# Performance work log

Hardware: AMD Instinct MI355X
Metric: run time of the kernel (lower is better)

## Reference

```python
import jax, jax.numpy as jnp
import numpy as np

B, S, HID = 4, 2048, 1024
NH, IM, E = 4, 2048, 4
EPS = 1e-6


def setup_inputs() -> dict:
    key = jax.random.key(0)
    ks = jax.random.split(key, 12)
    init = lambda k, shape: (jax.random.normal(k, shape, jnp.float32) * 0.02)
    return {
        "hidden_states": jax.random.normal(ks[0], (B, S, HID), jnp.float32),
        "ln1_w": jnp.ones((HID,), jnp.float32),
        "wq": init(ks[1], (HID, HID)),
        "wk": init(ks[2], (HID, HID)),
        "wv": init(ks[3], (HID, HID)),
        "wo": init(ks[4], (HID, HID)),
        "ln2_w": jnp.ones((HID,), jnp.float32),
        "router_w": init(ks[5], (HID, E)),
        "router_b": jnp.zeros((E,), jnp.float32),
        "gate_w": init(ks[6], (E, HID, IM)),
        "up_w": init(ks[7], (E, HID, IM)),
        "down_w": init(ks[8], (E, IM, HID)),
    }


def _rms(x, w):
    return w * (x * jax.lax.rsqrt(jnp.mean(x * x, axis=-1, keepdims=True) + EPS))


def reference(hidden_states, ln1_w, wq, wk, wv, wo, ln2_w,
              router_w, router_b, gate_w, up_w, down_w):
    b, s, h = hidden_states.shape
    nh, d = NH, h // NH

    # ---- attention block (elu+1 feature map, then full softmax) ----
    x = _rms(hidden_states, ln1_w)
    q = (x @ wq).reshape(b, s, nh, d).transpose(0, 2, 1, 3)  # [b,nh,s,d]
    k = (x @ wk).reshape(b, s, nh, d).transpose(0, 2, 1, 3)
    v = (x @ wv).reshape(b, s, nh, d).transpose(0, 2, 1, 3)
    q = jax.nn.elu(q) + 1.0
    k = jax.nn.elu(k) + 1.0
    scores = jnp.einsum('bhqd,bhkd->bhqk', q, k)
    attn = jax.nn.softmax(scores, axis=-1)  # dropout is identity at eval
    o = jnp.einsum('bhqk,bhkd->bhqd', attn, v)
    o = o.transpose(0, 2, 1, 3).reshape(b, s, h) @ wo
    h1 = hidden_states + o

    # ---- MoE block: router softmax, balance loss, dense expert loop ----
    x2 = _rms(h1, ln2_w)
    logits = x2 @ router_w + router_b            # [b,s,E]
    rw = jax.nn.softmax(logits, axis=-1)
    mean_routing = rw.mean(axis=0)               # mean over batch dim only, [s,E]
    balance_loss = jnp.mean((mean_routing - 1.0 / E) ** 2) * 0.01

    # source computes EVERY expert over all tokens, weighted by the FULL
    # softmax routing weight (top-k weights are computed but unused)
    moe_out = jnp.zeros_like(x2)
    for i in range(E):
        g = jax.nn.silu(x2 @ gate_w[i])
        u = x2 @ up_w[i]
        moe_out = moe_out + ((g * u) @ down_w[i]) * rw[..., i:i + 1]

    return h1 + moe_out, balance_loss
```

## Files before the change

### kernel.cpp

```cpp
#include <hip/hip_runtime.h>
#include <cstdint>
#include <cstddef>

#define B_    4
#define S_    2048
#define HID_  1024
#define NH_   4
#define HD_   256
#define IM_   2048
#define E_    4
#define M_    8192
#define NHG_  4

typedef __bf16 bf16x8 __attribute__((ext_vector_type(8)));
typedef float  f32x4  __attribute__((ext_vector_type(4)));

__device__ __forceinline__ unsigned short f32_to_bf16(float f) {
  unsigned int u = __float_as_uint(f);
  u += 0x7fffu + ((u >> 16) & 1u);
  return (unsigned short)(u >> 16);
}

__device__ __forceinline__ void gload16(const unsigned short* g, unsigned short* l) {
  __builtin_amdgcn_global_load_lds(
      (const __attribute__((address_space(1))) void*)g,
      (__attribute__((address_space(3))) void*)l, 16, 0, 0);
}

__device__ __forceinline__ void swizzle_xy(int& bx, int& by) {
  const int gx = gridDim.x, gy = gridDim.y;
  const int flat = blockIdx.x + blockIdx.y * gx;
  const int xcd = flat & 7, i = flat >> 3;
  const int rpx = gy >> 3;
  bx = i % gx;
  by = xcd * rpx + i / gx;
}

#define EPI_F32      0
#define EPI_VT       2
#define EPI_PV_O     3
#define EPI_WO       4
#define EPI_DOWN     5

struct EpiAux {
  float* c_f32;
  unsigned short* c_bf16;
  const float* add_src;
  float* out2;
  long long strideCz;
  int ldc;
};

template<int EPI>
__global__ __launch_bounds__(256) void gemm_bf16k(
    const unsigned short* __restrict__ A, int lda, long long sAo, long long sAi, int zbA,
    const unsigned short* __restrict__ B, int ldb, long long sBo, long long sBi, int zbB,
    int zshift, int zmask, int zbC, int K, EpiAux aux)
{
  __shared__ unsigned short As[2][128 * 32];
  __shared__ unsigned short Bs[2][128 * 32];

  const int t = threadIdx.x;
  int bx, by;
  swizzle_xy(bx, by);
  const int m0 = by * 128, n0 = bx * 128;
  const int z  = blockIdx.z;
  const int zA = z + zbA, zB = z + zbB, zC = z + zbC;
  const unsigned short* Ab = A + (long long)(zA >> zshift) * sAo + (long long)(zA & zmask) * sAi;
  const unsigned short* Bb = B + (long long)(zB >> zshift) * sBo + (long long)(zB & zmask) * sBi;

  const int lane = t & 63, wave = t >> 6;
  const int wm = (wave >> 1) * 64, wn = (wave & 1) * 64;
  const int lrow = lane & 15, quad = lane >> 4;

  f32x4 acc[4][4] = {};

  const int srow = lane >> 2;
  const int sko  = (lane & 3) * 8;
  const unsigned short* aRow0 = Ab + (long long)(m0 + wave * 16       + srow) * lda + sko;
  const unsigned short* aRow1 = Ab + (long long)(m0 + (wave + 4) * 16 + srow) * lda + sko;
  const unsigned short* bRow0 = Bb + (long long)(n0 + wave * 16       + srow) * ldb + sko;
  const unsigned short* bRow1 = Bb + (long long)(n0 + (wave + 4) * 16 + srow) * ldb + sko;
  const int dst0 = (wave * 16) * 32, dst1 = ((wave + 4) * 16) * 32;

  gload16(aRow0, &As[0][dst0]);
  gload16(aRow1, &As[0][dst1]);
  gload16(bRow0, &Bs[0][dst0]);
  gload16(bRow1, &Bs[0][dst1]);

  int cur = 0;
  for (int kk = 0; kk < K; kk += 32, cur ^= 1) {
    __syncthreads();
    if (kk + 32 < K) {
      const int nxt = cur ^ 1, k2 = kk + 32;
      gload16(aRow0 + k2, &As[nxt][dst0]);
      gload16(aRow1 + k2, &As[nxt][dst1]);
      gload16(bRow0 + k2, &Bs[nxt][dst0]);
      gload16(bRow1 + k2, &Bs[nxt][dst1]);
    }
    bf16x8 af[4], bfr[4];
    #pragma unroll
    for (int i = 0; i < 4; ++i) {
      af[i]  = *reinterpret_cast<const bf16x8*>(&As[cur][(wm + i * 16 + lrow) * 32 + quad * 8]);
      bfr[i] = *reinterpret_cast<const bf16x8*>(&Bs[cur][(wn + i * 16 + lrow) * 32 + quad * 8]);
    }
    #pragma unroll
    for (int i = 0; i < 4; ++i)
      #pragma unroll
      for (int j = 0; j < 4; ++j)
        acc[i][j] = __builtin_amdgcn_mfma_f32_16x16x32_bf16(af[i], bfr[j], acc[i][j], 0, 0, 0);
  }

  #pragma unroll
  for (int mi = 0; mi < 4; ++mi) {
    #pragma unroll
    for (int ni = 0; ni < 4; ++ni) {
      #pragma unroll
      for (int r = 0; r < 4; ++r) {
        const int gm = m0 + wm + mi * 16 + quad * 4 + r;
        const int gn = n0 + wn + ni * 16 + lrow;
        const float val = acc[mi][ni][r];
        if (EPI == EPI_F32) {
          aux.c_f32[(long long)zC * aux.strideCz + (long long)gm * aux.ldc + gn] = val;
        } else if (EPI == EPI_VT) {
          const int b = gm >> 11, s = gm & (S_ - 1);
          const int h = gn >> 8, d = gn & (HD_ - 1);
          aux.c_bf16[((long long)(b * NH_ + h) * HD_ + d) * S_ + s] = f32_to_bf16(val);
        } else if (EPI == EPI_PV_O) {
          const int b = zC >> 2, h = zC & (NH_ - 1);
          aux.c_bf16[((long long)(b * S_ + gm)) * HID_ + h * HD_ + gn] = f32_to_bf16(val);
        } else if (EPI == EPI_WO) {
          const long long idx = (long long)gm * HID_ + gn;
          aux.out2[idx] = val + aux.add_src[idx];
        } else if (EPI == EPI_DOWN) {
          const long long idx = (long long)gm * HID_ + gn;
          aux.out2[idx] += val;
        }
      }
    }
  }
}

#define EPI2_QK 0
#define EPI2_GU 1

template<int EPI2>
__global__ __launch_bounds__(256, 2) void gemm_dual_k(
    const unsigned short* __restrict__ A,
    const unsigned short* __restrict__ B0b,
    const unsigned short* __restrict__ B1b,
    int zb,
    unsigned short* __restrict__ out0, unsigned short* __restrict__ out1,
    const float* __restrict__ rw)
{
  __shared__ unsigned short As[2][128 * 32];
  __shared__ unsigned short B0s[2][128 * 32];
  __shared__ unsigned short B1s[2][128 * 32];

  const int t = threadIdx.x;
  int bx, by;
  swizzle_xy(bx, by);
  const int m0 = by * 128, n0 = bx * 128;

  const int lane = t & 63, wave = t >> 6;
  const int wm = (wave >> 1) * 64, wn = (wave & 1) * 64;
  const int lrow = lane & 15, quad = lane >> 4;

  f32x4 acc0[4][4] = {}, acc1[4][4] = {};

  const int srow = lane >> 2;
  const int sko  = (lane & 3) * 8;
  const unsigned short* aRow0 = A   + (long long)(m0 + wave * 16       + srow) * HID_ + sko;
  const unsigned short* aRow1 = A   + (long long)(m0 + (wave + 4) * 16 + srow) * HID_ + sko;
  const unsigned short* gRow0 = B0b + (long long)(n0 + wave * 16       + srow) * HID_ + sko;
  const unsigned short* gRow1 = B0b + (long long)(n0 + (wave + 4) * 16 + srow) * HID_ + sko;
  const unsigned short* uRow0 = B1b + (long long)(n0 + wave * 16       + srow) * HID_ + sko;
  const unsigned short* uRow1 = B1b + (long long)(n0 + (wave + 4) * 16 + srow) * HID_ + sko;
  const int dst0 = (wave * 16) * 32, dst1 = ((wave + 4) * 16) * 32;

  gload16(aRow0, &As[0][dst0]);
  gload16(aRow1, &As[0][dst1]);
  gload16(gRow0, &B0s[0][dst0]);
  gload16(gRow1, &B0s[0][dst1]);
  gload16(uRow0, &B1s[0][dst0]);
  gload16(uRow1, &B1s[0][dst1]);

  int cur = 0;
  for (int kk = 0; kk < HID_; kk += 32, cur ^= 1) {
    __syncthreads();
    if (kk + 32 < HID_) {
      const int nxt = cur ^ 1, k2 = kk + 32;
      gload16(aRow0 + k2, &As[nxt][dst0]);
      gload16(aRow1 + k2, &As[nxt][dst1]);
      gload16(gRow0 + k2, &B0s[nxt][dst0]);
      gload16(gRow1 + k2, &B0s[nxt][dst1]);
      gload16(uRow0 + k2, &B1s[nxt][dst0]);
      gload16(uRow1 + k2, &B1s[nxt][dst1]);
    }
    bf16x8 af[4], b0[4], b1[4];
    #pragma unroll
    for (int i = 0; i < 4; ++i) {
      af[i] = *reinterpret_cast<const bf16x8*>(&As[cur][(wm + i * 16 + lrow) * 32 + quad * 8]);
      b0[i] = *reinterpret_cast<const bf16x8*>(&B0s[cur][(wn + i * 16 + lrow) * 32 + quad * 8]);
      b1[i] = *reinterpret_cast<const bf16x8*>(&B1s[cur][(wn + i * 16 + lrow) * 32 + quad * 8]);
    }
    #pragma unroll
    for (int i = 0; i < 4; ++i)
      #pragma unroll
      for (int j = 0; j < 4; ++j) {
        acc0[i][j] = __builtin_amdgcn_mfma_f32_16x16x32_bf16(af[i], b0[j], acc0[i][j], 0, 0, 0);
        acc1[i][j] = __builtin_amdgcn_mfma_f32_16x16x32_bf16(af[i], b1[j], acc1[i][j], 0, 0, 0);
      }
  }

  #pragma unroll
  for (int mi = 0; mi < 4; ++mi)
    #pragma unroll
    for (int r = 0; r < 4; ++r) {
      const int gm = m0 + wm + mi * 16 + quad * 4 + r;
      float rwv = 0.f;
      if (EPI2 == EPI2_GU) rwv = rw[(long long)gm * E_ + zb];
      #pragma unroll
      for (int ni = 0; ni < 4; ++ni) {
        const int gn = n0 + wn + ni * 16 + lrow;
        const float v0 = acc0[mi][ni][r];
        const float v1 = acc1[mi][ni][r];
        if (EPI2 == EPI2_QK) {
          const float eq = v0 > 0.f ? v0 + 1.f : __expf(v0);
          const float ek = v1 > 0.f ? v1 + 1.f : __expf(v1);
          out0[(long long)gm * HID_ + gn] = f32_to_bf16(eq);
          out1[(long long)gm * HID_ + gn] = f32_to_bf16(ek);
        } else {
          const float sg = v0 / (1.f + __expf(-v0));
          out0[(long long)gm * IM_ + gn] = f32_to_bf16(sg * v1 * rwv);
        }
      }
    }
}

__global__ __launch_bounds__(256, 2) void gemm_down2_k(
    const unsigned short* __restrict__ A0,
    const unsigned short* __restrict__ A1,
    const unsigned short* __restrict__ B0,
    const unsigned short* __restrict__ B1,
    float* __restrict__ out)
{
  __shared__ unsigned short A0s[2][128 * 32];
  __shared__ unsigned short A1s[2][128 * 32];
  __shared__ unsigned short B0s[2][128 * 32];
  __shared__ unsigned short B1s[2][128 * 32];

  const int t = threadIdx.x;
  int bx, by;
  swizzle_xy(bx, by);
  const int m0 = by * 128, n0 = bx * 128;

  const int lane = t & 63, wave = t >> 6;
  const int wm = (wave >> 1) * 64, wn = (wave & 1) * 64;
  const int lrow = lane & 15, quad = lane >> 4;

  f32x4 acc[4][4] = {};

  const int srow = lane >> 2;
  const int sko  = (lane & 3) * 8;
  const unsigned short* a0r0 = A0 + (long long)(m0 + wave * 16       + srow) * IM_ + sko;
  const unsigned short* a0r1 = A0 + (long long)(m0 + (wave + 4) * 16 + srow) * IM_ + sko;
  const unsigned short* a1r0 = A1 + (long long)(m0 + wave * 16       + srow) * IM_ + sko;
  const unsigned short* a1r1 = A1 + (long long)(m0 + (wave + 4) * 16 + srow) * IM_ + sko;
  const unsigned short* b0r0 = B0 + (long long)(n0 + wave * 16       + srow) * IM_ + sko;
  const unsigned short* b0r1 = B0 + (long long)(n0 + (wave + 4) * 16 + srow) * IM_ + sko;
  const unsigned short* b1r0 = B1 + (long long)(n0 + wave * 16       + srow) * IM_ + sko;
  const unsigned short* b1r1 = B1 + (long long)(n0 + (wave + 4) * 16 + srow) * IM_ + sko;
  const int dst0 = (wave * 16) * 32, dst1 = ((wave + 4) * 16) * 32;

  gload16(a0r0, &A0s[0][dst0]);
  gload16(a0r1, &A0s[0][dst1]);
  gload16(a1r0, &A1s[0][dst0]);
  gload16(a1r1, &A1s[0][dst1]);
  gload16(b0r0, &B0s[0][dst0]);
  gload16(b0r1, &B0s[0][dst1]);
  gload16(b1r0, &B1s[0][dst0]);
  gload16(b1r1, &B1s[0][dst1]);

  int cur = 0;
  for (int kk = 0; kk < IM_; kk += 32, cur ^= 1) {
    __syncthreads();
    if (kk + 32 < IM_) {
      const int nxt = cur ^ 1, k2 = kk + 32;
      gload16(a0r0 + k2, &A0s[nxt][dst0]);
      gload16(a0r1 + k2, &A0s[nxt][dst1]);
      gload16(a1r0 + k2, &A1s[nxt][dst0]);
      gload16(a1r1 + k2, &A1s[nxt][dst1]);
      gload16(b0r0 + k2, &B0s[nxt][dst0]);
      gload16(b0r1 + k2, &B0s[nxt][dst1]);
      gload16(b1r0 + k2, &B1s[nxt][dst0]);
      gload16(b1r1 + k2, &B1s[nxt][dst1]);
    }
    bf16x8 a0f[4], a1f[4], b0f[4], b1f[4];
    #pragma unroll
    for (int i = 0; i < 4; ++i) {
      a0f[i] = *reinterpret_cast<const bf16x8*>(&A0s[cur][(wm + i * 16 + lrow) * 32 + quad * 8]);
      a1f[i] = *reinterpret_cast<const bf16x8*>(&A1s[cur][(wm + i * 16 + lrow) * 32 + quad * 8]);
      b0f[i] = *reinterpret_cast<const bf16x8*>(&B0s[cur][(wn + i * 16 + lrow) * 32 + quad * 8]);
      b1f[i] = *reinterpret_cast<const bf16x8*>(&B1s[cur][(wn + i * 16 + lrow) * 32 + quad * 8]);
    }
    #pragma unroll
    for (int i = 0; i < 4; ++i)
      #pragma unroll
      for (int j = 0; j < 4; ++j) {
        acc[i][j] = __builtin_amdgcn_mfma_f32_16x16x32_bf16(a0f[i], b0f[j], acc[i][j], 0, 0, 0);
        acc[i][j] = __builtin_amdgcn_mfma_f32_16x16x32_bf16(a1f[i], b1f[j], acc[i][j], 0, 0, 0);
      }
  }

  #pragma unroll
  for (int mi = 0; mi < 4; ++mi)
    #pragma unroll
    for (int ni = 0; ni < 4; ++ni)
      #pragma unroll
      for (int r = 0; r < 4; ++r) {
        const int gm = m0 + wm + mi * 16 + quad * 4 + r;
        const int gn = n0 + wn + ni * 16 + lrow;
        out[(long long)gm * HID_ + gn] += acc[mi][ni][r];
      }
}

__global__ void transpose_cast4_k(const float* s0, const float* s1,
                                  const float* s2, const float* s3,
                                  unsigned short* __restrict__ out, int R, int C)
{
  __shared__ float tile[32][33];
  const int z = blockIdx.z;
  const float* in = (z == 0) ? s0 : (z == 1) ? s1 : (z == 2) ? s2 : s3;
  unsigned short* o = out + (long long)z * R * C;
  const int c0 = blockIdx.x * 32, r0 = blockIdx.y * 32;
  const int tx = threadIdx.x, ty = threadIdx.y;
  #pragma unroll
  for (int i = 0; i < 32; i += 8)
    tile[ty + i][tx] = in[(long long)(r0 + ty + i) * C + c0 + tx];
  __syncthreads();
  #pragma unroll
  for (int i = 0; i < 32; i += 8)
    o[(long long)(c0 + ty + i) * R + r0 + tx] = f32_to_bf16(tile[tx][ty + i]);
}

__global__ void transpose_cast2x4_k(const float* __restrict__ sA,
                                    const float* __restrict__ sB,
                                    unsigned short* __restrict__ dA,
                                    unsigned short* __restrict__ dB,
                                    int R, int C)
{
  __shared__ float tile[32][33];
  const int z = blockIdx.z;
  const long long eo = (long long)(z & 3) * R * C;
  const float* in = ((z < 4) ? sA : sB) + eo;
  unsigned short* o = ((z < 4) ? dA : dB) + eo;
  const int c0 = blockIdx.x * 32, r0 = blockIdx.y * 32;
  const int tx = threadIdx.x, ty = threadIdx.y;
  #pragma unroll
  for (int i = 0; i < 32; i += 8)
    tile[ty + i][tx] = in[(long long)(r0 + ty + i) * C + c0 + tx];
  __syncthreads();
  #pragma unroll
  for (int i = 0; i < 32; i += 8)
    o[(long long)(c0 + ty + i) * R + r0 + tx] = f32_to_bf16(tile[tx][ty + i]);
}

__global__ void transpose_cast_k(const float* __restrict__ in,
                                 unsigned short* __restrict__ out, int R, int C)
{
  __shared__ float tile[32][33];
  const long long bo = (long long)blockIdx.z * R * C;
  const int c0 = blockIdx.x * 32, r0 = blockIdx.y * 32;
  const int tx = threadIdx.x, ty = threadIdx.y;
  #pragma unroll
  for (int i = 0; i < 32; i += 8)
    tile[ty + i][tx] = in[bo + (long long)(r0 + ty + i) * C + c0 + tx];
  __syncthreads();
  #pragma unroll
  for (int i = 0; i < 32; i += 8)
    out[bo + (long long)(c0 + ty + i) * R + r0 + tx] = f32_to_bf16(tile[tx][ty + i]);
}

__global__ __launch_bounds__(256) void rmsnorm_cast_k(
    const float* __restrict__ x, const float* __restrict__ w,
    unsigned short* __restrict__ out)
{
  __shared__ float red[4];
  const int row = blockIdx.x, t = threadIdx.x;
  const float4 v = reinterpret_cast<const float4*>(x + (long long)row * HID_)[t];
  float ss = v.x * v.x + v.y * v.y + v.z * v.z + v.w * v.w;
  #pragma unroll
  for (int off = 32; off > 0; off >>= 1) ss += __shfl_down(ss, off, 64);
  if ((t & 63) == 0) red[t >> 6] = ss;
  __syncthreads();
  ss = red[0] + red[1] + red[2] + red[3];
  const float inv = rsqrtf(ss * (1.0f / HID_) + 1e-6f);
  const float4 wv = reinterpret_cast<const float4*>(w)[t];
  ushort4 o;
  o.x = f32_to_bf16(v.x * inv * wv.x);
  o.y = f32_to_bf16(v.y * inv * wv.y);
  o.z = f32_to_bf16(v.z * inv * wv.z);
  o.w = f32_to_bf16(v.w * inv * wv.w);
  reinterpret_cast<ushort4*>(out + (long long)row * HID_)[t] = o;
}

__global__ __launch_bounds__(256) void softmax_rows_k(float* __restrict__ scores)
{
  __shared__ float red[4];
  const long long rbase = ((long long)blockIdx.y * S_ + blockIdx.x) * S_;
  float* row = scores + rbase;
  const int t = threadIdx.x;
  float v[8];
  #pragma unroll
  for (int i = 0; i < 8; ++i) v[i] = row[t + i * 256];
  float m = v[0];
  #pragma unroll
  for (int i = 1; i < 8; ++i) m = fmaxf(m, v[i]);
  #pragma unroll
  for (int off = 32; off > 0; off >>= 1) m = fmaxf(m, __shfl_down(m, off, 64));
  if ((t & 63) == 0) red[t >> 6] = m;
  __syncthreads();
  m = fmaxf(fmaxf(red[0], red[1]), fmaxf(red[2], red[3]));
  __syncthreads();
  float s = 0.f;
  #pragma unroll
  for (int i = 0; i < 8; ++i) { v[i] = __expf(v[i] - m); s += v[i]; }
  #pragma unroll
  for (int off = 32; off > 0; off >>= 1) s += __shfl_down(s, off, 64);
  if ((t & 63) == 0) red[t >> 6] = s;
  __syncthreads();
  const float inv = 1.0f / (red[0] + red[1] + red[2] + red[3]);
  unsigned short* prow = reinterpret_cast<unsigned short*>(scores) + rbase * 2;
  #pragma unroll
  for (int i = 0; i < 8; ++i) prow[t + i * 256] = f32_to_bf16(v[i] * inv);
}

__global__ __launch_bounds__(256) void router_k(
    const float* __restrict__ h1, const float* __restrict__ ln2w,
    const float* __restrict__ rwgt, const float* __restrict__ rbias,
    float* __restrict__ rw)
{
  const int wv = threadIdx.x >> 6, lane = threadIdx.x & 63;
  const long long m = (long long)blockIdx.x * 4 + wv;
  const float* xr = h1 + m * HID_;
  float xv[16];
  float ss = 0.f;
  #pragma unroll
  for (int i = 0; i < 16; ++i) { xv[i] = xr[lane + i * 64]; ss += xv[i] * xv[i]; }
  #pragma unroll
  for (int off = 32; off > 0; off >>= 1) ss += __shfl_down(ss, off, 64);
  ss = __shfl(ss, 0, 64);
  const float inv = rsqrtf(ss * (1.0f / HID_) + 1e-6f);
  float l0 = 0, l1 = 0, l2 = 0, l3 = 0;
  #pragma unroll
  for (int i = 0; i < 16; ++i) {
    const int k = lane + i * 64;
    const float xn = xv[i] * inv * ln2w[k];
    const float4 wr = reinterpret_cast<const float4*>(rwgt)[k];
    l0 += xn * wr.x; l1 += xn * wr.y; l2 += xn * wr.z; l3 += xn * wr.w;
  }
  #pragma unroll
  for (int off = 32; off > 0; off >>= 1) {
    l0 += __shfl_down(l0, off, 64);
    l1 += __shfl_down(l1, off, 64);
    l2 += __shfl_down(l2, off, 64);
    l3 += __shfl_down(l3, off, 64);
  }
  if (lane == 0) {
    l0 += rbias[0]; l1 += rbias[1]; l2 += rbias[2]; l3 += rbias[3];
    const float mx = fmaxf(fmaxf(l0, l1), fmaxf(l2, l3));
    const float e0 = __expf(l0 - mx), e1 = __expf(l1 - mx);
    const float e2 = __expf(l2 - mx), e3 = __expf(l3 - mx);
    const float is = 1.0f / (e0 + e1 + e2 + e3);
    reinterpret_cast<float4*>(rw)[m] = make_float4(e0 * is, e1 * is, e2 * is, e3 * is);
  }
}

__global__ __launch_bounds__(256) void balance_k(const float* __restrict__ rw,
                                                 float* __restrict__ out_scalar)
{
  __shared__ float red[4];
  float acc = 0.f;
  for (int it = threadIdx.x; it < S_ * E_; it += 256) {
    const int s = it >> 2, e = it & 3;
    float mr = 0.f;
    #pragma unroll
    for (int b = 0; b < B_; ++b) mr += rw[((long long)b * S_ + s) * E_ + e];
    mr *= (1.0f / B_);
    const float d = mr - 1.0f / E_;
    acc += d * d;
  }
  #pragma unroll
  for (int off = 32; off > 0; off >>= 1) acc += __shfl_down(acc, off, 64);
  if ((threadIdx.x & 63) == 0) red[threadIdx.x >> 6] = acc;
  __syncthreads();
  if (threadIdx.x == 0)
    out_scalar[0] = (red[0] + red[1] + red[2] + red[3]) * (0.01f / (S_ * E_));
}

extern "C" void kernel_launch(void* const* d_in, const int* in_sizes, int n_in,
                              void* d_out, int out_size, void* d_ws, size_t ws_size,
                              hipStream_t stream)
{
  const float* hidden   = (const float*)d_in[0];
  const float* ln1w     = (const float*)d_in[1];
  const float* wq       = (const float*)d_in[2];
  const float* wk       = (const float*)d_in[3];
  const float* wv       = (const float*)d_in[4];
  const float* wo       = (const float*)d_in[5];
  const float* ln2w     = (const float*)d_in[6];
  const float* router_w = (const float*)d_in[7];
  const float* router_b = (const float*)d_in[8];
  const float* gate_w   = (const float*)d_in[9];
  const float* up_w     = (const float*)d_in[10];
  const float* down_w   = (const float*)d_in[11];
  float* out = (float*)d_out;

  char* ws = (char*)d_ws;
  size_t off = 0;
  auto carve = [&](size_t bytes) {
    off = (off + 255) & ~(size_t)255;
    char* p = ws + off;
    off += bytes;
    return p;
  };
  unsigned short* wqT   = (unsigned short*)carve((size_t)HID_ * HID_ * 2);
  unsigned short* wkT   = (unsigned short*)carve((size_t)HID_ * HID_ * 2);
  unsigned short* wvT   = (unsigned short*)carve((size_t)HID_ * HID_ * 2);
  unsigned short* woT   = (unsigned short*)carve((size_t)HID_ * HID_ * 2);
  unsigned short* x_bf  = (unsigned short*)carve((size_t)M_ * HID_ * 2);
  unsigned short* qb    = (unsigned short*)carve((size_t)M_ * HID_ * 2);
  unsigned short* kb    = (unsigned short*)carve((size_t)M_ * HID_ * 2);
  unsigned short* vT    = (unsigned short*)carve((size_t)M_ * HID_ * 2);
  float*          rwbuf = (float*)carve((size_t)M_ * E_ * 4);
  char*           ubase = carve((size_t)NHG_ * S_ * S_ * 4);
  float*          scores = (float*)ubase;
  unsigned short* gateT = (unsigned short*)(ubase);
  unsigned short* upT   = (unsigned short*)(ubase + (size_t)16 * 1024 * 1024);
  unsigned short* downT = (unsigned short*)(ubase + (size_t)32 * 1024 * 1024);
  unsigned short* o_bf  = x_bf;
  unsigned short* x2_bf = qb;
  unsigned short* gu0   = kb;
  unsigned short* gu1   = (unsigned short*)carve((size_t)M_ * IM_ * 2);
  const bool paired = (ws_size >= off);

  const dim3 blk256(256), blkT(32, 8);

  transpose_cast4_k<<<dim3(32, 32, 4), blkT, 0, stream>>>(wq, wk, wv, wo, wqT, HID_, HID_);

  rmsnorm_cast_k<<<M_, blk256, 0, stream>>>(hidden, ln1w, x_bf);

  gemm_dual_k<EPI2_QK><<<dim3(8, 64, 1), blk256, 0, stream>>>(
      x_bf, wqT, wkT, 0, qb, kb, nullptr);
  {
    EpiAux a{}; a.c_bf16 = vT;
    gemm_bf16k<EPI_VT><<<dim3(8, 64, 1), blk256, 0, stream>>>(
        x_bf, HID_, 0, 0, 0, wvT, HID_, 0, 0, 0, 0, 0, 0, HID_, a);
  }

  for (int grp = 0; grp < 16 / NHG_; ++grp) {
    EpiAux as{}; as.c_f32 = scores; as.ldc = S_; as.strideCz = (long long)S_ * S_;
    gemm_bf16k<EPI_F32><<<dim3(16, 16, NHG_), blk256, 0, stream>>>(
        qb, HID_, (long long)S_ * HID_, HD_, grp * NHG_,
        kb, HID_, (long long)S_ * HID_, HD_, grp * NHG_,
        2, 3, 0, HD_, as);
    softmax_rows_k<<<dim3(S_, NHG_, 1), blk256, 0, stream>>>(scores);
    EpiAux ap{}; ap.c_bf16 = o_bf;
    gemm_bf16k<EPI_PV_O><<<dim3(2, 16, NHG_), blk256, 0, stream>>>(
        (const unsigned short*)scores, 2 * S_, (long long)S_ * 2 * S_, 0, 0,
        vT, S_, (long long)HD_ * S_, 0, grp * NHG_,
        0, 0, grp * NHG_, S_, ap);
  }

  transpose_cast2x4_k<<<dim3(64, 32, 8), blkT, 0, stream>>>(
      gate_w, up_w, gateT, upT, HID_, IM_);
  transpose_cast_k<<<dim3(32, 64, E_), blkT, 0, stream>>>(down_w, downT, IM_, HID_);

  {
    EpiAux a{}; a.add_src = hidden; a.out2 = out;
    gemm_bf16k<EPI_WO><<<dim3(8, 64, 1), blk256, 0, stream>>>(
        o_bf, HID_, 0, 0, 0, woT, HID_, 0, 0, 0, 0, 0, 0, HID_, a);
  }

  rmsnorm_cast_k<<<M_, blk256, 0, stream>>>(out, ln2w, x2_bf);
  router_k<<<M_ / 4, blk256, 0, stream>>>(out, ln2w, router_w, router_b, rwbuf);
  balance_k<<<1, blk256, 0, stream>>>(rwbuf, out + (size_t)M_ * HID_);

  const size_t wsz = (size_t)IM_ * HID_;
  if (paired) {
    for (int p = 0; p < 2; ++p) {
      const int e0 = 2 * p, e1 = e0 + 1;
      gemm_dual_k<EPI2_GU><<<dim3(16, 64, 1), blk256, 0, stream>>>(
          x2_bf, gateT + (size_t)e0 * wsz, upT + (size_t)e0 * wsz, e0, gu0, nullptr, rwbuf);
      gemm_dual_k<EPI2_GU><<<dim3(16, 64, 1), blk256, 0, stream>>>(
          x2_bf, gateT + (size_t)e1 * wsz, upT + (size_t)e1 * wsz, e1, gu1, nullptr, rwbuf);
      gemm_down2_k<<<dim3(8, 64, 1), blk256, 0, stream>>>(
          gu0, gu1, downT + (size_t)e0 * wsz, downT + (size_t)e1 * wsz, out);
    }
  } else {
    for (int i = 0; i < E_; ++i) {
      gemm_dual_k<EPI2_GU><<<dim3(16, 64, 1), blk256, 0, stream>>>(
          x2_bf, gateT + (size_t)i * wsz, upT + (size_t)i * wsz, i, gu0, nullptr, rwbuf);
      EpiAux ad{}; ad.out2 = out;
      gemm_bf16k<EPI_DOWN><<<dim3(8, 64, 1), blk256, 0, stream>>>(
          gu0, IM_, 0, 0, 0, downT + (size_t)i * wsz, IM_, 0, 0, 0,
          0, 0, 0, IM_, ad);
    }
  }
}
```

Measured before the change: 1.126 ms.

## Replace dual/down GEMMs with unified 512-thread triple-buffered swizzled GEMM

Adds a templated 512-thread GEMM with 256-wide N tiles, a three-stage LDS ring fed by direct global-to-LDS loads, XOR-swizzled LDS layout and explicit vmcnt waits. Gate/up and Q/K weights are interleaved in 16-row groups during the transpose, so a single B stream produces both outputs instead of two separate B tiles. This kernel replaces the QK, Wo, gate/up and paired-down GEMMs. It aims to raise MFMA density, cut LDS bank conflicts and hide load latency, at the cost of more LDS per block and hand-tuned wait counts that must match the load counts exactly.

```diff
diff --git a/kernel.cpp b/kernel.cpp
--- a/kernel.cpp
+++ b/kernel.cpp
@@ -27,6 +27,12 @@
       (__attribute__((address_space(3))) void*)l, 16, 0, 0);
 }
 
+template<int N> __device__ __forceinline__ void vwait() {
+  if constexpr (N == 0)      asm volatile("s_waitcnt vmcnt(0)" ::: "memory");
+  else if constexpr (N == 3) asm volatile("s_waitcnt vmcnt(3)" ::: "memory");
+  else                       asm volatile("s_waitcnt vmcnt(4)" ::: "memory");
+}
+
 __device__ __forceinline__ void swizzle_xy(int& bx, int& by) {
   const int gx = gridDim.x, gy = gridDim.y;
   const int flat = blockIdx.x + blockIdx.y * gx;
@@ -39,14 +45,10 @@
 #define EPI_F32      0
 #define EPI_VT       2
 #define EPI_PV_O     3
-#define EPI_WO       4
-#define EPI_DOWN     5
 
 struct EpiAux {
   float* c_f32;
   unsigned short* c_bf16;
-  const float* add_src;
-  float* out2;
   long long strideCz;
   int ldc;
 };
@@ -129,210 +131,169 @@
         } else if (EPI == EPI_PV_O) {
           const int b = zC >> 2, h = zC & (NH_ - 1);
           aux.c_bf16[((long long)(b * S_ + gm)) * HID_ + h * HD_ + gn] = f32_to_bf16(val);
-        } else if (EPI == EPI_WO) {
-          const long long idx = (long long)gm * HID_ + gn;
-          aux.out2[idx] = val + aux.add_src[idx];
-        } else if (EPI == EPI_DOWN) {
-          const long long idx = (long long)gm * HID_ + gn;
-          aux.out2[idx] += val;
         }
       }
     }
   }
 }
 
-#define EPI2_QK 0
-#define EPI2_GU 1
-
-template<int EPI2>
-__global__ __launch_bounds__(256, 2) void gemm_dual_k(
-    const unsigned short* __restrict__ A,
-    const unsigned short* __restrict__ B0b,
-    const unsigned short* __restrict__ B1b,
-    int zb,
-    unsigned short* __restrict__ out0, unsigned short* __restrict__ out1,
-    const float* __restrict__ rw)
-{
-  __shared__ unsigned short As[2][128 * 32];
-  __shared__ unsigned short B0s[2][128 * 32];
-  __shared__ unsigned short B1s[2][128 * 32];
-
-  const int t = threadIdx.x;
+#define EPI7_QK   0
+#define EPI7_GU   1
+#define EPI7_WO   2
+#define EPI7_DOWN 3
+template<int BM, int EPI, int KTOT, int KROW, bool PAIRK>
+__global__ __launch_bounds__(512, 2) void gemm7_k(
+    const unsigned short* A0, const unsigned short* A1,
+    const unsigned short* B0b, const unsigned short* B1b,
+    const float* __restrict__ rw, int expert,
+    unsigned short* out0, unsigned short* out1,
+    float* o_f32, const float* add_src)
+{
+  constexpr int NT    = KTOT / 32;
+  constexpr int NT2   = NT / 2;
+  constexpr int AU    = BM / 128;
+  constexpr int AELEM = BM * 32;
+  constexpr int LT    = AU + 2;
+  constexpr int MFR   = BM / 32;
+
+  __shared__ unsigned short smem[3 * AELEM + 3 * 8192];
+
+  const int t = threadIdx.x, wave = t >> 6, lane = t & 63;
+  const int lrow = lane & 15, quad = lane >> 4;
+  const int wrow0 = (wave >> 2) * (BM / 2);
+  const int wcol0 = (wave & 3) * 64;
+
   int bx, by;
   swizzle_xy(bx, by);
-  const int m0 = by * 128, n0 = bx * 128;
-
-  const int lane = t & 63, wave = t >> 6;
-  const int wm = (wave >> 1) * 64, wn = (wave & 1) * 64;
-  const int lrow = lane & 15, quad = lane >> 4;
-
-  f32x4 acc0[4][4] = {}, acc1[4][4] = {};
+  const int m0 = by * BM, n0 = bx * 256;
 
   const int srow = lane >> 2;
-  const int sko  = (lane & 3) * 8;
-  const unsigned short* aRow0 = A   + (long long)(m0 + wave * 16       + srow) * HID_ + sko;
-  const unsigned short* aRow1 = A   + (long long)(m0 + (wave + 4) * 16 + srow) * HID_ + sko;
-  const unsigned short* gRow0 = B0b + (long long)(n0 + wave * 16       + srow) * HID_ + sko;
-  const unsigned short* gRow1 = B0b + (long long)(n0 + (wave + 4) * 16 + srow) * HID_ + sko;
-  const unsigned short* uRow0 = B1b + (long long)(n0 + wave * 16       + srow) * HID_ + sko;
-  const unsigned short* uRow1 = B1b + (long long)(n0 + (wave + 4) * 16 + srow) * HID_ + sko;
-  const int dst0 = (wave * 16) * 32, dst1 = ((wave + 4) * 16) * 32;
-
-  gload16(aRow0, &As[0][dst0]);
-  gload16(aRow1, &As[0][dst1]);
-  gload16(gRow0, &B0s[0][dst0]);
-  gload16(gRow1, &B0s[0][dst1]);
-  gload16(uRow0, &B1s[0][dst0]);
-  gload16(uRow1, &B1s[0][dst1]);
-
-  int cur = 0;
-  for (int kk = 0; kk < HID_; kk += 32, cur ^= 1) {
-    __syncthreads();
-    if (kk + 32 < HID_) {
-      const int nxt = cur ^ 1, k2 = kk + 32;
-      gload16(aRow0 + k2, &As[nxt][dst0]);
-      gload16(aRow1 + k2, &As[nxt][dst1]);
-      gload16(gRow0 + k2, &B0s[nxt][dst0]);
-      gload16(gRow1 + k2, &B0s[nxt][dst1]);
-      gload16(uRow0 + k2, &B1s[nxt][dst0]);
-      gload16(uRow1 + k2, &B1s[nxt][dst1]);
-    }
-    bf16x8 af[4], b0[4], b1[4];
-    #pragma unroll
-    for (int i = 0; i < 4; ++i) {
-      af[i] = *reinterpret_cast<const bf16x8*>(&As[cur][(wm + i * 16 + lrow) * 32 + quad * 8]);
-      b0[i] = *reinterpret_cast<const bf16x8*>(&B0s[cur][(wn + i * 16 + lrow) * 32 + quad * 8]);
-      b1[i] = *reinterpret_cast<const bf16x8*>(&B1s[cur][(wn + i * 16 + lrow) * 32 + quad * 8]);
-    }
-    #pragma unroll
-    for (int i = 0; i < 4; ++i)
+  const int skb  = ((lane & 3) ^ (srow & 3)) << 4;
+  const char* pA[2]; const char* pB[2]; const char* qA[2]; const char* qB[2];
+  #pragma unroll
+  for (int u = 0; u < AU; ++u) {
+    const int row = m0 + u * 128 + wave * 16 + srow;
+    pA[u] = (const char*)(A0 + (size_t)row * KROW) + skb;
+    if constexpr (PAIRK) qA[u] = (const char*)(A1 + (size_t)row * KROW) + skb;
+  }
+  #pragma unroll
+  for (int u = 0; u < 2; ++u) {
+    const int row = n0 + u * 128 + wave * 16 + srow;
+    pB[u] = (const char*)(B0b + (size_t)row * KROW) + skb;
+    if constexpr (PAIRK) qB[u] = (const char*)(B1b + (size_t)row * KROW) + skb;
+  }
+
+  auto stage = [&](int sb) {
+    #pragma unroll
+    for (int u = 0; u < AU; ++u) {
+      gload16((const unsigned short*)pA[u], &smem[sb * AELEM + u * 4096 + wave * 512]);
+      pA[u] += 64;
+    }
+    #pragma unroll
+    for (int u = 0; u < 2; ++u) {
+      gload16((const unsigned short*)pB[u], &smem[3 * AELEM + sb * 8192 + u * 4096 + wave * 512]);
+      pB[u] += 64;
+    }
+  };
+
+  int roA[MFR], roB[4];
+  const int swz = (quad ^ (lrow & 3)) << 4;
+  #pragma unroll
+  for (int mi = 0; mi < MFR; ++mi)
+    roA[mi] = (wrow0 + mi * 16 + lrow) * 64 + swz;
+  #pragma unroll
+  for (int nj = 0; nj < 4; ++nj)
+    roB[nj] = (wcol0 + nj * 16 + lrow) * 64 + swz;
+
+  f32x4 acc[MFR][4] = {};
+
+  stage(0);
+  stage(1);
+
+  int rd = 0, sb = 2;
+  for (int T = 0; T < NT; ++T) {
+    if constexpr (PAIRK) {
+      if (T + 2 == NT2) {
+        #pragma unroll
+        for (int u = 0; u < AU; ++u) pA[u] = qA[u];
+        pB[0] = qB[0]; pB[1] = qB[1];
+      }
+    }
+    if (T == NT - 1)      vwait<0>();
+    else if (LT == 4)     vwait<4>();
+    else                  vwait<3>();
+    __builtin_amdgcn_s_barrier();
+    __builtin_amdgcn_sched_barrier(0);
+    if (T + 2 < NT) stage(sb);
+
+    const char* aB = (const char*)smem + rd * (AELEM * 2);
+    const char* bB = (const char*)smem + 3 * AELEM * 2 + rd * 16384;
+    bf16x8 bf[4];
+    #pragma unroll
+    for (int nj = 0; nj < 4; ++nj)
+      bf[nj] = *(const bf16x8*)(bB + roB[nj]);
+    #pragma unroll
+    for (int h = 0; h < MFR / 4; ++h) {
+      bf16x8 af[4];
       #pragma unroll
-      for (int j = 0; j < 4; ++j) {
-        acc0[i][j] = __builtin_amdgcn_mfma_f32_16x16x32_bf16(af[i], b0[j], acc0[i][j], 0, 0, 0);
-        acc1[i][j] = __builtin_amdgcn_mfma_f32_16x16x32_bf16(af[i], b1[j], acc1[i][j], 0, 0, 0);
-      }
-  }
-
-  #pragma unroll
-  for (int mi = 0; mi < 4; ++mi)
+      for (int i = 0; i < 4; ++i)
+        af[i] = *(const bf16x8*)(aB + roA[h * 4 + i]);
+      __builtin_amdgcn_s_setprio(1);
+      #pragma unroll
+      for (int i = 0; i < 4; ++i)
+        #pragma unroll
+        for (int nj = 0; nj < 4; ++nj)
+          acc[h * 4 + i][nj] =
+              __builtin_amdgcn_mfma_f32_16x16x32_bf16(af[i], bf[nj], acc[h * 4 + i][nj], 0, 0, 0);
+      __builtin_amdgcn_s_setprio(0);
+    }
+    if (++rd == 3) rd = 0;
+    if (++sb == 3) sb = 0;
+  }
+
+  #pragma unroll
+  for (int mi = 0; mi < MFR; ++mi) {
     #pragma unroll
     for (int r = 0; r < 4; ++r) {
-      const int gm = m0 + wm + mi * 16 + quad * 4 + r;
+      const int gm = m0 + wrow0 + mi * 16 + quad * 4 + r;
       float rwv = 0.f;
-      if (EPI2 == EPI2_GU) rwv = rw[(long long)gm * E_ + zb];
-      #pragma unroll
-      for (int ni = 0; ni < 4; ++ni) {
-        const int gn = n0 + wn + ni * 16 + lrow;
-        const float v0 = acc0[mi][ni][r];
-        const float v1 = acc1[mi][ni][r];
-        if (EPI2 == EPI2_QK) {
-          const float eq = v0 > 0.f ? v0 + 1.f : __expf(v0);
-          const float ek = v1 > 0.f ? v1 + 1.f : __expf(v1);
-          out0[(long long)gm * HID_ + gn] = f32_to_bf16(eq);
-          out1[(long long)gm * HID_ + gn] = f32_to_bf16(ek);
-        } else {
-          const float sg = v0 / (1.f + __expf(-v0));
-          out0[(long long)gm * IM_ + gn] = f32_to_bf16(sg * v1 * rwv);
+      if (EPI == EPI7_GU) rwv = rw[(size_t)gm * E_ + expert];
+      if (EPI == EPI7_QK || EPI == EPI7_GU) {
+        #pragma unroll
+        for (int pj = 0; pj < 2; ++pj) {
+          const int col = ((n0 + wcol0) >> 1) + pj * 16 + lrow;
+          const float v0 = acc[mi][2 * pj][r];
+          const float v1 = acc[mi][2 * pj + 1][r];
+          if (EPI == EPI7_QK) {
+            out0[(size_t)gm * HID_ + col] = f32_to_bf16(v0 > 0.f ? v0 + 1.f : __expf(v0));
+            out1[(size_t)gm * HID_ + col] = f32_to_bf16(v1 > 0.f ? v1 + 1.f : __expf(v1));
+          } else {
+            const float sg = v0 / (1.f + __expf(-v0));
+            out0[(size_t)gm * IM_ + col] = f32_to_bf16(sg * v1 * rwv);
+          }
+        }
+      } else {
+        #pragma unroll
+        for (int nj = 0; nj < 4; ++nj) {
+          const int gn = n0 + wcol0 + nj * 16 + lrow;
+          const size_t idx = (size_t)gm * HID_ + gn;
+          if (EPI == EPI7_WO) o_f32[idx] = acc[mi][nj][r] + add_src[idx];
+          else                o_f32[idx] += acc[mi][nj][r];
         }
       }
     }
-}
-
-__global__ __launch_bounds__(256, 2) void gemm_down2_k(
-    const unsigned short* __restrict__ A0,
-    const unsigned short* __restrict__ A1,
-    const unsigned short* __restrict__ B0,
-    const unsigned short* __restrict__ B1,
-    float* __restrict__ out)
-{
-  __shared__ unsigned short A0s[2][128 * 32];
-  __shared__ unsigned short A1s[2][128 * 32];
-  __shared__ unsigned short B0s[2][128 * 32];
-  __shared__ unsigned short B1s[2][128 * 32];
-
-  const int t = threadIdx.x;
-  int bx, by;
-  swizzle_xy(bx, by);
-  const int m0 = by * 128, n0 = bx * 128;
-
-  const int lane = t & 63, wave = t >> 6;
-  const int wm = (wave >> 1) * 64, wn = (wave & 1) * 64;
-  const int lrow = lane & 15, quad = lane >> 4;
-
-  f32x4 acc[4][4] = {};
-
-  const int srow = lane >> 2;
-  const int sko  = (lane & 3) * 8;
-  const unsigned short* a0r0 = A0 + (long long)(m0 + wave * 16       + srow) * IM_ + sko;
-  const unsigned short* a0r1 = A0 + (long long)(m0 + (wave + 4) * 16 + srow) * IM_ + sko;
-  const unsigned short* a1r0 = A1 + (long long)(m0 + wave * 16       + srow) * IM_ + sko;
-  const unsigned short* a1r1 = A1 + (long long)(m0 + (wave + 4) * 16 + srow) * IM_ + sko;
-  const unsigned short* b0r0 = B0 + (long long)(n0 + wave * 16       + srow) * IM_ + sko;
-  const unsigned short* b0r1 = B0 + (long long)(n0 + (wave + 4) * 16 + srow) * IM_ + sko;
-  const unsigned short* b1r0 = B1 + (long long)(n0 + wave * 16       + srow) * IM_ + sko;
-  const unsigned short* b1r1 = B1 + (long long)(n0 + (wave + 4) * 16 + srow) * IM_ + sko;
-  const int dst0 = (wave * 16) * 32, dst1 = ((wave + 4) * 16) * 32;
-
-  gload16(a0r0, &A0s[0][dst0]);
-  gload16(a0r1, &A0s[0][dst1]);
-  gload16(a1r0, &A1s[0][dst0]);
-  gload16(a1r1, &A1s[0][dst1]);
-  gload16(b0r0, &B0s[0][dst0]);
-  gload16(b0r1, &B0s[0][dst1]);
-  gload16(b1r0, &B1s[0][dst0]);
-  gload16(b1r1, &B1s[0][dst1]);
-
-  int cur = 0;
-  for (int kk = 0; kk < IM_; kk += 32, cur ^= 1) {
-    __syncthreads();
-    if (kk + 32 < IM_) {
-      const int nxt = cur ^ 1, k2 = kk + 32;
-      gload16(a0r0 + k2, &A0s[nxt][dst0]);
-      gload16(a0r1 + k2, &A0s[nxt][dst1]);
-      gload16(a1r0 + k2, &A1s[nxt][dst0]);
-      gload16(a1r1 + k2, &A1s[nxt][dst1]);
-      gload16(b0r0 + k2, &B0s[nxt][dst0]);
-      gload16(b0r1 + k2, &B0s[nxt][dst1]);
-      gload16(b1r0 + k2, &B1s[nxt][dst0]);
-      gload16(b1r1 + k2, &B1s[nxt][dst1]);
-    }
-    bf16x8 a0f[4], a1f[4], b0f[4], b1f[4];
-    #pragma unroll
-    for (int i = 0; i < 4; ++i) {
-      a0f[i] = *reinterpret_cast<const bf16x8*>(&A0s[cur][(wm + i * 16 + lrow) * 32 + quad * 8]);
-      a1f[i] = *reinterpret_cast<const bf16x8*>(&A1s[cur][(wm + i * 16 + lrow) * 32 + quad * 8]);
-      b0f[i] = *reinterpret_cast<const bf16x8*>(&B0s[cur][(wn + i * 16 + lrow) * 32 + quad * 8]);
-      b1f[i] = *reinterpret_cast<const bf16x8*>(&B1s[cur][(wn + i * 16 + lrow) * 32 + quad * 8]);
-    }
-    #pragma unroll
-    for (int i = 0; i < 4; ++i)
-      #pragma unroll
-      for (int j = 0; j < 4; ++j) {
-        acc[i][j] = __builtin_amdgcn_mfma_f32_16x16x32_bf16(a0f[i], b0f[j], acc[i][j], 0, 0, 0);
-        acc[i][j] = __builtin_amdgcn_mfma_f32_16x16x32_bf16(a1f[i], b1f[j], acc[i][j], 0, 0, 0);
-      }
-  }
-
-  #pragma unroll
-  for (int mi = 0; mi < 4; ++mi)
-    #pragma unroll
-    for (int ni = 0; ni < 4; ++ni)
-      #pragma unroll
-      for (int r = 0; r < 4; ++r) {
-        const int gm = m0 + wm + mi * 16 + quad * 4 + r;
-        const int gn = n0 + wn + ni * 16 + lrow;
-        out[(long long)gm * HID_ + gn] += acc[mi][ni][r];
-      }
+  }
 }
 
 __global__ void transpose_cast4_k(const float* s0, const float* s1,
                                   const float* s2, const float* s3,
-                                  unsigned short* __restrict__ out, int R, int C)
+                                  unsigned short* __restrict__ qkT,
+                                  unsigned short* __restrict__ vT,
+                                  unsigned short* __restrict__ woT, int R, int C)
 {
   __shared__ float tile[32][33];
   const int z = blockIdx.z;
   const float* in = (z == 0) ? s0 : (z == 1) ? s1 : (z == 2) ? s2 : s3;
-  unsigned short* o = out + (long long)z * R * C;
   const int c0 = blockIdx.x * 32, r0 = blockIdx.y * 32;
   const int tx = threadIdx.x, ty = threadIdx.y;
   #pragma unroll
@@ -340,21 +301,31 @@
     tile[ty + i][tx] = in[(long long)(r0 + ty + i) * C + c0 + tx];
   __syncthreads();
   #pragma unroll
-  for (int i = 0; i < 32; i += 8)
-    o[(long long)(c0 + ty + i) * R + r0 + tx] = f32_to_bf16(tile[tx][ty + i]);
+  for (int i = 0; i < 32; i += 8) {
+    const int c = c0 + ty + i;
+    const unsigned short v = f32_to_bf16(tile[tx][ty + i]);
+    if (z < 2) {
+      const int orow = ((c >> 4) << 5) + (c & 15) + (z << 4);
+      qkT[(long long)orow * R + r0 + tx] = v;
+    } else if (z == 2) {
+      vT[(long long)c * R + r0 + tx] = v;
+    } else {
+      woT[(long long)c * R + r0 + tx] = v;
+    }
+  }
 }
 
 __global__ void transpose_cast2x4_k(const float* __restrict__ sA,
                                     const float* __restrict__ sB,
-                                    unsigned short* __restrict__ dA,
-                                    unsigned short* __restrict__ dB,
+                                    unsigned short* __restrict__ guT,
                                     int R, int C)
 {
   __shared__ float tile[32][33];
   const int z = blockIdx.z;
   const long long eo = (long long)(z & 3) * R * C;
   const float* in = ((z < 4) ? sA : sB) + eo;
-  unsigned short* o = ((z < 4) ? dA : dB) + eo;
+  unsigned short* o = guT + (long long)(z & 3) * 2 * R * C;
+  const int par16 = (z < 4) ? 0 : 16;
   const int c0 = blockIdx.x * 32, r0 = blockIdx.y * 32;
   const int tx = threadIdx.x, ty = threadIdx.y;
   #pragma unroll
@@ -362,8 +333,11 @@
     tile[ty + i][tx] = in[(long long)(r0 + ty + i) * C + c0 + tx];
   __syncthreads();
   #pragma unroll
-  for (int i = 0; i < 32; i += 8)
-    o[(long long)(c0 + ty + i) * R + r0 + tx] = f32_to_bf16(tile[tx][ty + i]);
+  for (int i = 0; i < 32; i += 8) {
+    const int c = c0 + ty + i;
+    const int orow = ((c >> 4) << 5) + (c & 15) + par16;
+    o[(long long)orow * R + r0 + tx] = f32_to_bf16(tile[tx][ty + i]);
+  }
 }
 
 __global__ void transpose_cast_k(const float* __restrict__ in,
@@ -525,8 +499,7 @@
     off += bytes;
     return p;
   };
-  unsigned short* wqT   = (unsigned short*)carve((size_t)HID_ * HID_ * 2);
-  unsigned short* wkT   = (unsigned short*)carve((size_t)HID_ * HID_ * 2);
+  unsigned short* qkT   = (unsigned short*)carve((size_t)2 * HID_ * HID_ * 2);
   unsigned short* wvT   = (unsigned short*)carve((size_t)HID_ * HID_ * 2);
   unsigned short* woT   = (unsigned short*)carve((size_t)HID_ * HID_ * 2);
   unsigned short* x_bf  = (unsigned short*)carve((size_t)M_ * HID_ * 2);
@@ -536,8 +509,7 @@
   float*          rwbuf = (float*)carve((size_t)M_ * E_ * 4);
   char*           ubase = carve((size_t)NHG_ * S_ * S_ * 4);
   float*          scores = (float*)ubase;
-  unsigned short* gateT = (unsigned short*)(ubase);
-  unsigned short* upT   = (unsigned short*)(ubase + (size_t)16 * 1024 * 1024);
+  unsigned short* guT   = (unsigned short*)(ubase);
   unsigned short* downT = (unsigned short*)(ubase + (size_t)32 * 1024 * 1024);
   unsigned short* o_bf  = x_bf;
   unsigned short* x2_bf = qb;
@@ -545,14 +517,15 @@
   unsigned short* gu1   = (unsigned short*)carve((size_t)M_ * IM_ * 2);
   const bool paired = (ws_size >= off);
 
-  const dim3 blk256(256), blkT(32, 8);
-
-  transpose_cast4_k<<<dim3(32, 32, 4), blkT, 0, stream>>>(wq, wk, wv, wo, wqT, HID_, HID_);
+  const dim3 blk256(256), blk512(512), blkT(32, 8);
+
+  transpose_cast4_k<<<dim3(32, 32, 4), blkT, 0, stream>>>(
+      wq, wk, wv, wo, qkT, wvT, woT, HID_, HID_);
 
   rmsnorm_cast_k<<<M_, blk256, 0, stream>>>(hidden, ln1w, x_bf);
 
-  gemm_dual_k<EPI2_QK><<<dim3(8, 64, 1), blk256, 0, stream>>>(
-      x_bf, wqT, wkT, 0, qb, kb, nullptr);
+  gemm7_k<256, EPI7_QK, 1024, 1024, false><<<dim3(8, 32, 1), blk512, 0, stream>>>(
+      x_bf, nullptr, qkT, nullptr, nullptr, 0, qb, kb, nullptr, nullptr);
   {
     EpiAux a{}; a.c_bf16 = vT;
     gemm_bf16k<EPI_VT><<<dim3(8, 64, 1), blk256, 0, stream>>>(
@@ -574,38 +547,39 @@
   }
 
   transpose_cast2x4_k<<<dim3(64, 32, 8), blkT, 0, stream>>>(
-      gate_w, up_w, gateT, upT, HID_, IM_);
+      gate_w, up_w, guT, HID_, IM_);
   transpose_cast_k<<<dim3(32, 64, E_), blkT, 0, stream>>>(down_w, downT, IM_, HID_);
 
-  {
-    EpiAux a{}; a.add_src = hidden; a.out2 = out;
-    gemm_bf16k<EPI_WO><<<dim3(8, 64, 1), blk256, 0, stream>>>(
-        o_bf, HID_, 0, 0, 0, woT, HID_, 0, 0, 0, 0, 0, 0, HID_, a);
-  }
+  gemm7_k<128, EPI7_WO, 1024, 1024, false><<<dim3(4, 64, 1), blk512, 0, stream>>>(
+      o_bf, nullptr, woT, nullptr, nullptr, 0, nullptr, nullptr, out, hidden);
 
   rmsnorm_cast_k<<<M_, blk256, 0, stream>>>(out, ln2w, x2_bf);
   router_k<<<M_ / 4, blk256, 0, stream>>>(out, ln2w, router_w, router_b, rwbuf);
   balance_k<<<1, blk256, 0, stream>>>(rwbuf, out + (size_t)M_ * HID_);
 
+  const size_t w2 = (size_t)2 * IM_ * HID_;
   const size_t wsz = (size_t)IM_ * HID_;
   if (paired) {
     for (int p = 0; p < 2; ++p) {
       const int e0 = 2 * p, e1 = e0 + 1;
-      gemm_dual_k<EPI2_GU><<<dim3(16, 64, 1), blk256, 0, stream>>>(
-          x2_bf, gateT + (size_t)e0 * wsz, upT + (size_t)e0 * wsz, e0, gu0, nullptr, rwbuf);
-      gemm_dual_k<EPI2_GU><<<dim3(16, 64, 1), blk256, 0, stream>>>(
-          x2_bf, gateT + (size_t)e1 * wsz, upT + (size_t)e1 * wsz, e1, gu1, nullptr, rwbuf);
-      gemm_down2_k<<<dim3(8, 64, 1), blk256, 0, stream>>>(
-          gu0, gu1, downT + (size_t)e0 * wsz, downT + (size_t)e1 * wsz, out);
+      gemm7_k<256, EPI7_GU, 1024, 1024, false><<<dim3(16, 32, 1), blk512, 0, stream>>>(
+          x2_bf, nullptr, guT + (size_t)e0 * w2, nullptr,
+          rwbuf, e0, gu0, nullptr, nullptr, nullptr);
+      gemm7_k<256, EPI7_GU, 1024, 1024, false><<<dim3(16, 32, 1), blk512, 0, stream>>>(
+          x2_bf, nullptr, guT + (size_t)e1 * w2, nullptr,
+          rwbuf, e1, gu1, nullptr, nullptr, nullptr);
+      gemm7_k<128, EPI7_DOWN, 4096, 2048, true><<<dim3(4, 64, 1), blk512, 0, stream>>>(
+          gu0, gu1, downT + (size_t)e0 * wsz, downT + (size_t)e1 * wsz,
+          nullptr, 0, nullptr, nullptr, out, nullptr);
     }
   } else {
     for (int i = 0; i < E_; ++i) {
-      gemm_dual_k<EPI2_GU><<<dim3(16, 64, 1), blk256, 0, stream>>>(
-          x2_bf, gateT + (size_t)i * wsz, upT + (size_t)i * wsz, i, gu0, nullptr, rwbuf);
-      EpiAux ad{}; ad.out2 = out;
-      gemm_bf16k<EPI_DOWN><<<dim3(8, 64, 1), blk256, 0, stream>>>(
-          gu0, IM_, 0, 0, 0, downT + (size_t)i * wsz, IM_, 0, 0, 0,
-          0, 0, 0, IM_, ad);
-    }
-  }
-}
+      gemm7_k<256, EPI7_GU, 1024, 1024, false><<<dim3(16, 32, 1), blk512, 0, stream>>>(
+          x2_bf, nullptr, guT + (size_t)i * w2, nullptr,
+          rwbuf, i, gu0, nullptr, nullptr, nullptr);
+      gemm7_k<128, EPI7_DOWN, 2048, 2048, false><<<dim3(4, 64, 1), blk512, 0, stream>>>(
+          gu0, nullptr, downT + (size_t)i * wsz, nullptr,
+          nullptr, 0, nullptr, nullptr, out, nullptr);
+    }
+  }
+}
```

New measurement: 1.091 ms. -3.1%, faster.
